# Kernel tuning notes

Measured on AMD Instinct MI355X. Metric: run time of the kernel, lower is better.

## Reference

```python
import jax, jax.numpy as jnp
import numpy as np

BATCH, N_NODES = 256, 128
NF = MF = 128
EF = AEF = 5


def setup_inputs() -> dict:
    key = jax.random.key(0)
    k = jax.random.split(key, 6)
    afm = jax.random.normal(k[0], (BATCH, N_NODES, NF), dtype=jnp.float32)
    bfm = jax.random.randint(k[1], (BATCH, N_NODES, N_NODES), 0, EF + 1, dtype=jnp.int32)
    a_bfm = jax.random.randint(k[2], (BATCH, N_NODES), 0, AEF + 1, dtype=jnp.int32)
    adj = jax.random.uniform(k[3], (BATCH, N_NODES, N_NODES), dtype=jnp.float32)
    # xavier_uniform for adj_w (ef, mf, nf): fan_in=nf, fan_out=mf per torch convention on last two dims
    lim_w = float(np.sqrt(6.0 / (MF + NF)))
    adj_w = jax.random.uniform(k[4], (EF, MF, NF), minval=-lim_w, maxval=lim_w, dtype=jnp.float32)
    lim_a = float(np.sqrt(6.0 / (AEF + MF)))
    adj_a = jax.random.uniform(k[5], (AEF, MF), minval=-lim_a, maxval=lim_a, dtype=jnp.float32)
    return {"afm": afm, "bfm": bfm, "a_bfm": a_bfm, "adj": adj, "adj_w": adj_w, "adj_a": adj_a}


def reference(afm, bfm, a_bfm, adj, adj_w, adj_a):
    # afm is accepted by the original forward but never used.
    E = adj_w.shape[0] + 1  # zeros row for "no edge" at index 0
    mf, nf = adj_w.shape[1], adj_w.shape[2]
    W_ext = jnp.concatenate([jnp.zeros((1, mf, nf), adj_w.dtype), adj_w], axis=0)  # (E, mf, nf)
    A_ext = jnp.concatenate([jnp.zeros((1, mf), adj_a.dtype), adj_a], axis=0)      # (E_a, mf)
    att = A_ext[a_bfm]  # (b, n, mf); nf == mf required by original matmul
    # Original: msg[b,i,j,m] = sum_k W_ext[bfm[b,i,j], m, k] * att[b, j, k], then sum over i.
    # Contract first per edge type (small), then count-weight instead of gathering huge tensor.
    contrib = jnp.einsum('emn,bjn->bjem', W_ext, att)                  # (b, n, E, mf)
    cnt = jax.nn.one_hot(bfm, E, dtype=contrib.dtype).sum(axis=1)      # (b, j, E) = #{i : bfm[b,i,j]=e}
    messages = jnp.einsum('bje,bjem->bjm', cnt, contrib)               # (b, n, mf)
    return jnp.matmul(adj, messages)                                   # (b, n, mf)
```

## Files before the change

kernel.cpp:

```cpp
#include <hip/hip_runtime.h>

typedef short s16x8 __attribute__((ext_vector_type(8)));
typedef float f32x4 __attribute__((ext_vector_type(4)));

__device__ __forceinline__ short f2bf(float f) {
  union { float f; unsigned u; } cv;
  cv.f = f;
  unsigned u = cv.u;
  u = (u + 0x7FFFu + ((u >> 16) & 1u)) >> 16;
  return (short)u;
}
__device__ __forceinline__ unsigned pk2(float lo, float hi) {
  union { float f; unsigned u; } a, b;
  a.f = lo;
  b.f = hi;
  return (a.u >> 16) | (b.u & 0xFFFF0000u);
}

__global__ __launch_bounds__(256, 4) void hist_mc_kernel(
    const int* __restrict__ bfm, const float* __restrict__ adj_w,
    const float* __restrict__ adj_a, uint2* __restrict__ cnt_g,
    unsigned short* __restrict__ McT) {
  __shared__ unsigned red[4][8][4][2];
  __shared__ float As[5][128];
  const int t = threadIdx.x;

  if (blockIdx.x >= 1024) {
    const int bi = blockIdx.x - 1024;
    const int e = bi >> 2, mg = bi & 3;
    for (int idx = t; idx < 640; idx += 256) As[idx >> 7][idx & 127] = adj_a[idx];
    __syncthreads();
    const int m = mg * 32 + (t >> 3), ns = t & 7;
    const float* W = adj_w + (size_t)e * 16384 + (size_t)m * 128 + ns * 16;
    float acc[5] = {0.f, 0.f, 0.f, 0.f, 0.f};
#pragma unroll
    for (int it = 0; it < 4; ++it) {
      const float4 wv = *(const float4*)(W + it * 4);
      const float wa[4] = {wv.x, wv.y, wv.z, wv.w};
#pragma unroll
      for (int q = 0; q < 4; ++q) {
        const int n = ns * 16 + it * 4 + q;
#pragma unroll
        for (int a = 0; a < 5; ++a) acc[a] = fmaf(wa[q], As[a][n], acc[a]);
      }
    }
#pragma unroll
    for (int d = 1; d < 8; d <<= 1)
#pragma unroll
      for (int a = 0; a < 5; ++a) acc[a] += __shfl_xor(acc[a], d);
    if (ns == 0) {
#pragma unroll
      for (int a = 0; a < 5; ++a)
        McT[m * 40 + e * 5 + a] = (unsigned short)f2bf(acc[a]);
      if (e == 0)
#pragma unroll
        for (int r = 25; r < 40; ++r) McT[m * 40 + r] = 0;
    }
    return;
  }

  const int b = blockIdx.x >> 2, jg = blockIdx.x & 3;
  const int w = t >> 6, l = t & 63, c4 = l & 7, rr = l >> 3;
  const int4* bp = (const int4*)bfm + (size_t)b * 4096 + jg * 8 + c4;
  unsigned pA[4] = {0, 0, 0, 0}, pB[4] = {0, 0, 0, 0};
#pragma unroll
  for (int it = 0; it < 4; ++it) {
    const int i = it * 32 + w * 8 + rr;
    const int4 v = bp[(size_t)i * 32];
    const int vv[4] = {v.x, v.y, v.z, v.w};
#pragma unroll
    for (int jj = 0; jj < 4; ++jj) {
      pA[jj] += (unsigned)(vv[jj] == 1) + ((unsigned)(vv[jj] == 2) << 8) +
                ((unsigned)(vv[jj] == 3) << 16) + ((unsigned)(vv[jj] == 4) << 24);
      pB[jj] += (unsigned)(vv[jj] == 5);
    }
  }
#pragma unroll
  for (int d = 8; d < 64; d <<= 1)
#pragma unroll
    for (int jj = 0; jj < 4; ++jj) {
      pA[jj] += (unsigned)__shfl_xor((int)pA[jj], d);
      pB[jj] += (unsigned)__shfl_xor((int)pB[jj], d);
    }
  if (rr == 0)
#pragma unroll
    for (int jj = 0; jj < 4; ++jj) {
      red[w][c4][jj][0] = pA[jj];
      red[w][c4][jj][1] = pB[jj];
    }
  __syncthreads();
  if (t < 32) {
    unsigned A = 0, B = 0;
    const int cc = t >> 2, jj = t & 3;
#pragma unroll
    for (int w2 = 0; w2 < 4; ++w2) {
      A += red[w2][cc][jj][0];
      B += red[w2][cc][jj][1];
    }
    cnt_g[b * 128 + jg * 32 + t] = make_uint2(A, B);
  }
}

__global__ __launch_bounds__(128, 3) void skinny_kernel(
    const float* __restrict__ adj, const int* __restrict__ a_bfm,
    const uint2* __restrict__ cnt_g, const unsigned short* __restrict__ McT,
    float* __restrict__ out) {
  __shared__ __align__(16) unsigned short Pt[32 * 128];
  __shared__ __align__(16) unsigned short Mt[128 * 40];
  __shared__ __align__(16) unsigned short Qs[2 * 16 * 40];
  const int bq = blockIdx.x, b = bq >> 2, qq = bq & 3;
  const int t = threadIdx.x, w = t >> 6, l = t & 63, g = l >> 4, c = l & 15;
  const int row0 = qq * 32 + w * 16;

  const uint2 cc2 = cnt_g[b * 128 + t];
  const int av = a_bfm[b * 128 + t];
  s16x8 mst[5];
#pragma unroll
  for (int i = 0; i < 5; ++i) mst[i] = *(const s16x8*)&McT[(i * 128 + t) * 8];
  const float* arow = adj + (size_t)b * 16384 + (size_t)(row0 + c) * 128;
  float4 a0[4], a1[4];
#pragma unroll
  for (int kk = 0; kk < 4; ++kk) {
    a0[kk] = *(const float4*)(arow + kk * 32 + g * 8);
    a1[kk] = *(const float4*)(arow + kk * 32 + g * 8 + 4);
  }

#pragma unroll
  for (int i = 0; i < 4; ++i)
    ((uint4*)Pt)[i * 128 + t] = make_uint4(0u, 0u, 0u, 0u);
#pragma unroll
  for (int i = 0; i < 5; ++i) *(s16x8*)&Mt[(i * 128 + t) * 8] = mst[i];
  asm volatile("s_waitcnt lgkmcnt(0)" ::: "memory");
  __builtin_amdgcn_s_barrier();

  if (av > 0) {
    const int ai = av - 1;
    const int chunk = t >> 3, off = t & 7;
    const float cf[5] = {(float)(cc2.x & 255u), (float)((cc2.x >> 8) & 255u),
                         (float)((cc2.x >> 16) & 255u), (float)(cc2.x >> 24),
                         (float)(cc2.y & 255u)};
#pragma unroll
    for (int ei = 0; ei < 5; ++ei) {
      const int r = ei * 5 + ai;
      Pt[r * 128 + ((chunk ^ (r & 15)) << 3) + off] =
          (unsigned short)f2bf(cf[ei]);
    }
  }
  asm volatile("s_waitcnt lgkmcnt(0)" ::: "memory");
  __builtin_amdgcn_s_barrier();

  s16x8 bP[4][2];
#pragma unroll
  for (int kk = 0; kk < 4; ++kk)
#pragma unroll
    for (int ct = 0; ct < 2; ++ct) {
      const int r = ct * 16 + c;
      bP[kk][ct] = *(const s16x8*)&Pt[r * 128 + (((kk * 4 + g) ^ (r & 15)) << 3)];
    }
  s16x8 apk[4];
#pragma unroll
  for (int kk = 0; kk < 4; ++kk) {
    unsigned* pu = (unsigned*)&apk[kk];
    pu[0] = pk2(a0[kk].x, a0[kk].y);
    pu[1] = pk2(a0[kk].z, a0[kk].w);
    pu[2] = pk2(a1[kk].x, a1[kk].y);
    pu[3] = pk2(a1[kk].z, a1[kk].w);
  }
  f32x4 accQ[2] = {{0.f, 0.f, 0.f, 0.f}, {0.f, 0.f, 0.f, 0.f}};
#pragma unroll
  for (int kk = 0; kk < 4; ++kk)
#pragma unroll
    for (int ct = 0; ct < 2; ++ct)
      accQ[ct] =
          __builtin_amdgcn_mfma_f32_16x16x32_bf16(apk[kk], bP[kk][ct], accQ[ct], 0, 0, 0);

  unsigned short* qsw = &Qs[w * 16 * 40];
#pragma unroll
  for (int ct = 0; ct < 2; ++ct)
#pragma unroll
    for (int q = 0; q < 4; ++q)
      qsw[(g * 4 + q) * 40 + ct * 16 + c] = (unsigned short)f2bf(accQ[ct][q]);
  const s16x8 aQ = *(const s16x8*)&qsw[c * 40 + g * 8];

  float* ob = out + (size_t)b * 16384 + (size_t)row0 * 128;
#pragma unroll
  for (int mt = 0; mt < 8; ++mt) {
    const s16x8 bM = *(const s16x8*)&Mt[(mt * 16 + c) * 40 + g * 8];
    f32x4 acc2 = {0.f, 0.f, 0.f, 0.f};
    acc2 = __builtin_amdgcn_mfma_f32_16x16x32_bf16(aQ, bM, acc2, 0, 0, 0);
#pragma unroll
    for (int q = 0; q < 4; ++q)
      ob[(g * 4 + q) * 128 + mt * 16 + c] = acc2[q];
  }
}

extern "C" void kernel_launch(void* const* d_in, const int* in_sizes, int n_in,
                              void* d_out, int out_size, void* d_ws,
                              size_t ws_size, hipStream_t stream) {
  const int* bfm = (const int*)d_in[1];
  const int* a_bfm = (const int*)d_in[2];
  const float* adj = (const float*)d_in[3];
  const float* adj_w = (const float*)d_in[4];
  const float* adj_a = (const float*)d_in[5];
  float* out = (float*)d_out;

  unsigned short* McT = (unsigned short*)d_ws;
  uint2* cnt_g = (uint2*)((char*)d_ws + 16384);

  hist_mc_kernel<<<dim3(1044), dim3(256), 0, stream>>>(bfm, adj_w, adj_a,
                                                       cnt_g, McT);
  skinny_kernel<<<dim3(1024), dim3(128), 0, stream>>>(adj, a_bfm, cnt_g, McT,
                                                      out);
}
```

Measured before the change: 17.86 us.

## Split histogram by row halves and use larger blocks in both kernels

The histogram kernel now assigns each block half of a batch's rows across all 128 columns, reading bfm contiguously instead of strided column groups. Each block writes partial counts that the second kernel adds together. The second kernel now uses 256-thread blocks covering 64 output rows, so each batch needs half as many blocks and the staging loads of the counts and McT are shared more widely. The McT blocks are moved to the front of the grid. The aim is better coalescing and less per-block overhead, at the cost of an extra partial-count read and lower occupancy bounds.

```diff
diff --git a/kernel.cpp b/kernel.cpp
--- a/kernel.cpp
+++ b/kernel.cpp
@@ -19,14 +19,14 @@
 
 __global__ __launch_bounds__(256, 4) void hist_mc_kernel(
     const int* __restrict__ bfm, const float* __restrict__ adj_w,
-    const float* __restrict__ adj_a, uint2* __restrict__ cnt_g,
+    const float* __restrict__ adj_a, uint2* __restrict__ cnt_h,
     unsigned short* __restrict__ McT) {
-  __shared__ unsigned red[4][8][4][2];
+  __shared__ unsigned red[4][32][4][2];
   __shared__ float As[5][128];
   const int t = threadIdx.x;
 
-  if (blockIdx.x >= 1024) {
-    const int bi = blockIdx.x - 1024;
+  if (blockIdx.x < 20) {
+    const int bi = blockIdx.x;
     const int e = bi >> 2, mg = bi & 3;
     for (int idx = t; idx < 640; idx += 256) As[idx >> 7][idx & 127] = adj_a[idx];
     __syncthreads();
@@ -59,14 +59,14 @@
     return;
   }
 
-  const int b = blockIdx.x >> 2, jg = blockIdx.x & 3;
-  const int w = t >> 6, l = t & 63, c4 = l & 7, rr = l >> 3;
-  const int4* bp = (const int4*)bfm + (size_t)b * 4096 + jg * 8 + c4;
+  const int idx2 = blockIdx.x - 20;
+  const int b = idx2 >> 1, hh = idx2 & 1;
+  const int w = t >> 6, l = t & 63;
+  const int4* bp = (const int4*)bfm + (size_t)b * 4096 + hh * 2048;
   unsigned pA[4] = {0, 0, 0, 0}, pB[4] = {0, 0, 0, 0};
 #pragma unroll
-  for (int it = 0; it < 4; ++it) {
-    const int i = it * 32 + w * 8 + rr;
-    const int4 v = bp[(size_t)i * 32];
+  for (int it = 0; it < 8; ++it) {
+    const int4 v = bp[it * 256 + t];
     const int vv[4] = {v.x, v.y, v.z, v.w};
 #pragma unroll
     for (int jj = 0; jj < 4; ++jj) {
@@ -76,20 +76,19 @@
     }
   }
 #pragma unroll
-  for (int d = 8; d < 64; d <<= 1)
+  for (int jj = 0; jj < 4; ++jj) {
+    pA[jj] += (unsigned)__shfl_xor((int)pA[jj], 32);
+    pB[jj] += (unsigned)__shfl_xor((int)pB[jj], 32);
+  }
+  if (l < 32) {
 #pragma unroll
     for (int jj = 0; jj < 4; ++jj) {
-      pA[jj] += (unsigned)__shfl_xor((int)pA[jj], d);
-      pB[jj] += (unsigned)__shfl_xor((int)pB[jj], d);
-    }
-  if (rr == 0)
-#pragma unroll
-    for (int jj = 0; jj < 4; ++jj) {
-      red[w][c4][jj][0] = pA[jj];
-      red[w][c4][jj][1] = pB[jj];
-    }
+      red[w][l][jj][0] = pA[jj];
+      red[w][l][jj][1] = pB[jj];
+    }
+  }
   __syncthreads();
-  if (t < 32) {
+  if (t < 128) {
     unsigned A = 0, B = 0;
     const int cc = t >> 2, jj = t & 3;
 #pragma unroll
@@ -97,26 +96,32 @@
       A += red[w2][cc][jj][0];
       B += red[w2][cc][jj][1];
     }
-    cnt_g[b * 128 + jg * 32 + t] = make_uint2(A, B);
-  }
-}
-
-__global__ __launch_bounds__(128, 3) void skinny_kernel(
+    cnt_h[(b * 2 + hh) * 128 + t] = make_uint2(A, B);
+  }
+}
+
+__global__ __launch_bounds__(256, 2) void skinny_kernel(
     const float* __restrict__ adj, const int* __restrict__ a_bfm,
-    const uint2* __restrict__ cnt_g, const unsigned short* __restrict__ McT,
+    const uint2* __restrict__ cnt_h, const unsigned short* __restrict__ McT,
     float* __restrict__ out) {
   __shared__ __align__(16) unsigned short Pt[32 * 128];
   __shared__ __align__(16) unsigned short Mt[128 * 40];
-  __shared__ __align__(16) unsigned short Qs[2 * 16 * 40];
-  const int bq = blockIdx.x, b = bq >> 2, qq = bq & 3;
+  __shared__ __align__(16) unsigned short Qs[4 * 16 * 40];
+  const int bh = blockIdx.x, b = bh >> 1, hh = bh & 1;
   const int t = threadIdx.x, w = t >> 6, l = t & 63, g = l >> 4, c = l & 15;
-  const int row0 = qq * 32 + w * 16;
-
-  const uint2 cc2 = cnt_g[b * 128 + t];
-  const int av = a_bfm[b * 128 + t];
-  s16x8 mst[5];
-#pragma unroll
-  for (int i = 0; i < 5; ++i) mst[i] = *(const s16x8*)&McT[(i * 128 + t) * 8];
+  const int row0 = hh * 64 + w * 16;
+
+  uint2 h0 = make_uint2(0u, 0u), h1 = make_uint2(0u, 0u);
+  int av = 0;
+  if (t < 128) {
+    h0 = cnt_h[(b * 2 + 0) * 128 + t];
+    h1 = cnt_h[(b * 2 + 1) * 128 + t];
+    av = a_bfm[b * 128 + t];
+  }
+  s16x8 mst0 = *(const s16x8*)&McT[t * 8];
+  s16x8 mst1 = *(const s16x8*)&McT[(256 + t) * 8];
+  s16x8 mst2 = {0, 0, 0, 0, 0, 0, 0, 0};
+  if (t < 128) mst2 = *(const s16x8*)&McT[(512 + t) * 8];
   const float* arow = adj + (size_t)b * 16384 + (size_t)(row0 + c) * 128;
   float4 a0[4], a1[4];
 #pragma unroll
@@ -126,19 +131,22 @@
   }
 
 #pragma unroll
-  for (int i = 0; i < 4; ++i)
-    ((uint4*)Pt)[i * 128 + t] = make_uint4(0u, 0u, 0u, 0u);
-#pragma unroll
-  for (int i = 0; i < 5; ++i) *(s16x8*)&Mt[(i * 128 + t) * 8] = mst[i];
+  for (int i = 0; i < 2; ++i)
+    ((uint4*)Pt)[i * 256 + t] = make_uint4(0u, 0u, 0u, 0u);
+  *(s16x8*)&Mt[t * 8] = mst0;
+  *(s16x8*)&Mt[(256 + t) * 8] = mst1;
+  if (t < 128) *(s16x8*)&Mt[(512 + t) * 8] = mst2;
   asm volatile("s_waitcnt lgkmcnt(0)" ::: "memory");
   __builtin_amdgcn_s_barrier();
 
-  if (av > 0) {
+  if (t < 128 && av > 0) {
+    const unsigned cx = h0.x + h1.x;
+    const unsigned cy = h0.y + h1.y;
     const int ai = av - 1;
     const int chunk = t >> 3, off = t & 7;
-    const float cf[5] = {(float)(cc2.x & 255u), (float)((cc2.x >> 8) & 255u),
-                         (float)((cc2.x >> 16) & 255u), (float)(cc2.x >> 24),
-                         (float)(cc2.y & 255u)};
+    const float cf[5] = {(float)(cx & 255u), (float)((cx >> 8) & 255u),
+                         (float)((cx >> 16) & 255u), (float)(cx >> 24),
+                         (float)(cy & 255u)};
 #pragma unroll
     for (int ei = 0; ei < 5; ++ei) {
       const int r = ei * 5 + ai;
@@ -171,8 +179,8 @@
   for (int kk = 0; kk < 4; ++kk)
 #pragma unroll
     for (int ct = 0; ct < 2; ++ct)
-      accQ[ct] =
-          __builtin_amdgcn_mfma_f32_16x16x32_bf16(apk[kk], bP[kk][ct], accQ[ct], 0, 0, 0);
+      accQ[ct] = __builtin_amdgcn_mfma_f32_16x16x32_bf16(apk[kk], bP[kk][ct],
+                                                         accQ[ct], 0, 0, 0);
 
   unsigned short* qsw = &Qs[w * 16 * 40];
 #pragma unroll
@@ -205,10 +213,10 @@
   float* out = (float*)d_out;
 
   unsigned short* McT = (unsigned short*)d_ws;
-  uint2* cnt_g = (uint2*)((char*)d_ws + 16384);
-
-  hist_mc_kernel<<<dim3(1044), dim3(256), 0, stream>>>(bfm, adj_w, adj_a,
-                                                       cnt_g, McT);
-  skinny_kernel<<<dim3(1024), dim3(128), 0, stream>>>(adj, a_bfm, cnt_g, McT,
-                                                      out);
-}
+  uint2* cnt_h = (uint2*)((char*)d_ws + 16384);
+
+  hist_mc_kernel<<<dim3(532), dim3(256), 0, stream>>>(bfm, adj_w, adj_a,
+                                                      cnt_h, McT);
+  skinny_kernel<<<dim3(512), dim3(256), 0, stream>>>(adj, a_bfm, cnt_h, McT,
+                                                     out);
+}
```

Result: faster. 17.08 us (-4.3%).
